# Kernel tuning notes

Measured on AMD Instinct MI355X. Metric: run time of the kernel, lower is better.

Reference implementation:

```python
import jax, jax.numpy as jnp
import numpy as np

N_NODES = 100000
N_EDGES = 100000
NNZ = 1600000


def setup_inputs() -> dict:
    key = jax.random.key(0)
    ks = jax.random.split(key, 6)
    x = jax.random.normal(ks[0], (N_NODES, 128), dtype=jnp.float32)
    hyperedge_index = jax.random.randint(ks[1], (2, NNZ), 0, N_EDGES, dtype=jnp.int64)
    # Glorot-ish init for linear weights, zero bias (PyG HypergraphConv lin + bias)
    W1 = jax.random.normal(ks[2], (128, 128), dtype=jnp.float32) / np.sqrt(128.0)
    b1 = jnp.zeros((128,), dtype=jnp.float32)
    W2 = jax.random.normal(ks[3], (128, 64), dtype=jnp.float32) / np.sqrt(128.0)
    b2 = jnp.zeros((64,), dtype=jnp.float32)
    return {"x": x, "hyperedge_index": hyperedge_index, "W1": W1, "b1": b1, "W2": W2, "b2": b2}


def _hypergraph_conv(x, node_idx, edge_idx, W, b):
    """PyG HypergraphConv (no attention, unit hyperedge weights):
    out = D^{-1} H B^{-1} H^T (x W) + b, with D = node degree, B = hyperedge degree."""
    x = x @ W  # [N, F]
    ones = jnp.ones((node_idx.shape[0],), dtype=x.dtype)
    deg_v = jax.ops.segment_sum(ones, node_idx, num_segments=N_NODES)   # D
    deg_e = jax.ops.segment_sum(ones, edge_idx, num_segments=N_EDGES)   # B
    d_inv = jnp.where(deg_v > 0, 1.0 / deg_v, 0.0)
    b_inv = jnp.where(deg_e > 0, 1.0 / deg_e, 0.0)
    # node -> hyperedge: m_e = B_e^{-1} * sum_{v in e} x_v
    m_e = jax.ops.segment_sum(x[node_idx], edge_idx, num_segments=N_EDGES) * b_inv[:, None]
    # hyperedge -> node: out_v = D_v^{-1} * sum_{e ∋ v} m_e
    out = jax.ops.segment_sum(m_e[edge_idx], node_idx, num_segments=N_NODES) * d_inv[:, None]
    return out + b


def reference(x, hyperedge_index, W1, b1, W2, b2):
    node_idx = hyperedge_index[0]
    edge_idx = hyperedge_index[1]
    h = _hypergraph_conv(x, node_idx, edge_idx, W1, b1)
    h = jax.nn.relu(h)
    # dropout is identity in eval mode (training=False)
    out = _hypergraph_conv(h, node_idx, edge_idx, W2, b2)
    return out
```

## Files before the change

kernel.cpp:

```cpp
#include <hip/hip_runtime.h>

#define NODES 100000
#define EDGES 100000
#define NNZV  1600000
#define NBK   196
#define BKCAP 12288
#define TILE2 2048
#define NTIL2 782

typedef unsigned short u16;
typedef __attribute__((ext_vector_type(8))) short bf16x8;
typedef __attribute__((ext_vector_type(4))) float f32x4;

__device__ __forceinline__ float b2f(u16 h) {
  union { unsigned u; float f; } c; c.u = ((unsigned)h) << 16; return c.f;
}
__device__ __forceinline__ u16 f2b(float f) {
  union { unsigned u; float f; } c; c.f = f;
  unsigned u = c.u + 0x7FFF + ((c.u >> 16) & 1);
  return (u16)(u >> 16);
}

__global__ __launch_bounds__(256) void wtrans_kernel(const float* __restrict__ W1,
                                                     const float* __restrict__ W2,
                                                     u16* __restrict__ W1T, u16* __restrict__ W2T) {
  int i = blockIdx.x * 256 + threadIdx.x;
  if (i < 16384) {
    int k = i >> 7, n = i & 127;
    W1T[n * 128 + k] = f2b(W1[i]);
  } else if (i < 16384 + 8192) {
    int j = i - 16384;
    int k = j >> 6, n = j & 63;
    W2T[n * 128 + k] = f2b(W2[j]);
  }
}

__global__ __launch_bounds__(256) void partition_kernel(const int* __restrict__ nidx,
                                                        const int* __restrict__ eidx,
                                                        int* __restrict__ gcnt,
                                                        unsigned* __restrict__ bk) {
  __shared__ int lcnt_e[NBK], lcnt_n[NBK], lbase_e[NBK], lbase_n[NBK];
  const int tid = threadIdx.x;
  const int j0 = blockIdx.x * TILE2;
  for (int i = tid; i < NBK; i += 256) { lcnt_e[i] = 0; lcnt_n[i] = 0; }
  __syncthreads();
  int be[8], bn[8]; unsigned pe[8], pn[8];
  #pragma unroll
  for (int i = 0; i < 8; i++) {
    int j = j0 + tid + i * 256;
    if (j < NNZV) {
      int e = __builtin_nontemporal_load(eidx + j);
      int n = __builtin_nontemporal_load(nidx + j);
      be[i] = e >> 9; pe[i] = ((unsigned)(e & 511) << 17) | (unsigned)n;
      bn[i] = n >> 9; pn[i] = ((unsigned)(n & 511) << 17) | (unsigned)e;
      atomicAdd(&lcnt_e[be[i]], 1);
      atomicAdd(&lcnt_n[bn[i]], 1);
    } else { be[i] = -1; bn[i] = -1; }
  }
  __syncthreads();
  for (int b = tid; b < NBK; b += 256) {
    int c = lcnt_e[b];
    lbase_e[b] = c ? atomicAdd(&gcnt[b], c) : 0;
    lcnt_e[b] = 0;
    c = lcnt_n[b];
    lbase_n[b] = c ? atomicAdd(&gcnt[NBK + b], c) : 0;
    lcnt_n[b] = 0;
  }
  __syncthreads();
  #pragma unroll
  for (int i = 0; i < 8; i++) {
    if (be[i] >= 0) {
      int p = lbase_e[be[i]] + atomicAdd(&lcnt_e[be[i]], 1);
      if (p < BKCAP) bk[(size_t)be[i] * BKCAP + p] = pe[i];
      p = lbase_n[bn[i]] + atomicAdd(&lcnt_n[bn[i]], 1);
      if (p < BKCAP) bk[(size_t)(NBK + bn[i]) * BKCAP + p] = pn[i];
    }
  }
}

__global__ __launch_bounds__(512) void bucket_sort_kernel(const int* __restrict__ gcnt,
                                                          const unsigned* __restrict__ bk,
                                                          int* __restrict__ off_e, int* __restrict__ off_v,
                                                          int* __restrict__ col_e, int* __restrict__ col_v) {
  const int gb = blockIdx.x;
  const int dir = gb >= NBK ? 1 : 0;
  const int b = dir ? gb - NBK : gb;
  const int* __restrict__ cnt = gcnt + dir * NBK;
  const unsigned* __restrict__ bkd = bk + ((size_t)dir * NBK + b) * BKCAP;
  int* __restrict__ off = dir ? off_v : off_e;
  int* __restrict__ col = dir ? col_v : col_e;
  const int tid = threadIdx.x, lane = tid & 63, wid = tid >> 6;
  __shared__ int lcnt[512];
  __shared__ int wsum[8];
  __shared__ int base_s;
  if (tid < 64) {
    int s = 0;
    for (int t = tid; t < b; t += 64) s += cnt[t];
    #pragma unroll
    for (int d = 1; d < 64; d <<= 1) s += __shfl_xor(s, d);
    if (tid == 0) base_s = s;
  }
  lcnt[tid] = 0;
  __syncthreads();
  const int n = min(cnt[b], BKCAP);
  for (int i = tid; i < n; i += 512)
    atomicAdd(&lcnt[bkd[i] >> 17], 1);
  __syncthreads();
  int x = lcnt[tid];
  int inc = x;
  #pragma unroll
  for (int d = 1; d < 64; d <<= 1) { int t = __shfl_up(inc, d); if (lane >= d) inc += t; }
  if (lane == 63) wsum[wid] = inc;
  __syncthreads();
  int wbase = 0;
  for (int k = 0; k < wid; k++) wbase += wsum[k];
  const int gpos = base_s + wbase + inc - x;
  const int row = (b << 9) + tid;
  if (row < NODES) off[row] = gpos;
  if (b == NBK - 1 && tid == 0) off[NODES] = NNZV;
  __syncthreads();
  lcnt[tid] = gpos;
  __syncthreads();
  for (int i = tid; i < n; i += 512) {
    unsigned e = bkd[i];
    int p = atomicAdd(&lcnt[e >> 17], 1);
    col[p] = (int)(e & 0x1FFFFu);
  }
}

template<int N, bool XBF>
__global__ __launch_bounds__(256) void gemm_kernel(const void* __restrict__ Xv,
                                                   const u16* __restrict__ WT,
                                                   u16* __restrict__ Y, int M) {
  __shared__ u16 sX[64 * 136];
  __shared__ u16 sW[N * 136];
  const int tid = threadIdx.x, lane = tid & 63, w = tid >> 6;
  const int chunk = blockIdx.x * 64;
  constexpr int WV = N * 128 / 8;
  for (int t = tid; t < WV; t += 256) {
    int e = t * 8, n = e >> 7, k = e & 127;
    *(bf16x8*)(sW + n * 136 + k) = *(const bf16x8*)(WT + n * 128 + k);
  }
  if constexpr (XBF) {
    const u16* X = (const u16*)Xv;
    for (int t = tid; t < 1024; t += 256) {
      int e = t * 8, r = e >> 7, k = e & 127;
      int row = min(chunk + r, M - 1);
      *(bf16x8*)(sX + r * 136 + k) = *(const bf16x8*)(X + (size_t)row * 128 + k);
    }
  } else {
    const float* X = (const float*)Xv;
    for (int t = tid; t < 2048; t += 256) {
      int r = t >> 5, c4 = t & 31;
      int row = min(chunk + r, M - 1);
      float4 v = *(const float4*)(X + (size_t)row * 128 + c4 * 4);
      ushort4 o = { f2b(v.x), f2b(v.y), f2b(v.z), f2b(v.w) };
      *(ushort4*)(sX + r * 136 + c4 * 4) = o;
    }
  }
  __syncthreads();
  constexpr int CW = N / 2;
  constexpr int NT = CW / 16;
  const int wr = w >> 1, wc = w & 1;
  const int l15 = lane & 15;
  const int arow = wr * 32 + l15;
  const int kb = (lane >> 4) * 8;
  f32x4 acc[2][NT];
  #pragma unroll
  for (int rt = 0; rt < 2; rt++)
    #pragma unroll
    for (int nt = 0; nt < NT; nt++) acc[rt][nt] = (f32x4){0.f, 0.f, 0.f, 0.f};
  #pragma unroll
  for (int kk = 0; kk < 4; kk++) {
    const int ko = kk * 32 + kb;
    bf16x8 a0 = *(const bf16x8*)(sX + arow * 136 + ko);
    bf16x8 a1 = *(const bf16x8*)(sX + (arow + 16) * 136 + ko);
    #pragma unroll
    for (int nt = 0; nt < NT; nt++) {
      bf16x8 bb = *(const bf16x8*)(sW + (wc * CW + nt * 16 + l15) * 136 + ko);
      acc[0][nt] = __builtin_amdgcn_mfma_f32_16x16x32_bf16(a0, bb, acc[0][nt], 0, 0, 0);
      acc[1][nt] = __builtin_amdgcn_mfma_f32_16x16x32_bf16(a1, bb, acc[1][nt], 0, 0, 0);
    }
  }
  const int r4 = (lane >> 4) * 4;
  #pragma unroll
  for (int rt = 0; rt < 2; rt++)
    #pragma unroll
    for (int r = 0; r < 4; r++) {
      int row = chunk + wr * 32 + rt * 16 + r4 + r;
      if (row < M) {
        #pragma unroll
        for (int nt = 0; nt < NT; nt++)
          Y[(size_t)row * N + wc * CW + nt * 16 + l15] = f2b(acc[rt][nt][r]);
      }
    }
}

template<int F, bool HASB, bool RELU, bool DSTBF>
__global__ __launch_bounds__(256) void gather_kernel(const int* __restrict__ off,
                                                     const int* __restrict__ col,
                                                     const u16* __restrict__ src,
                                                     const float* __restrict__ bias,
                                                     void* __restrict__ dstv, int nrows) {
  constexpr int G = (F == 128) ? 4 : 8;
  constexpr int L = 64 / G;
  const int row = blockIdx.x * 4 + (threadIdx.x >> 6);
  if (row >= nrows) return;
  const int lane = threadIdx.x & 63;
  const int g = lane / L;
  const int l = lane % L;
  const int s0 = off[row], s1 = off[row + 1];
  float acc[8] = {};
  int k = s0;
  for (; k + 4 * G <= s1; k += 4 * G) {
    int c0 = col[k + g];
    int c1 = col[k + G + g];
    int c2 = col[k + 2 * G + g];
    int c3 = col[k + 3 * G + g];
    bf16x8 v0 = *(const bf16x8*)(src + (size_t)c0 * F + l * 8);
    bf16x8 v1 = *(const bf16x8*)(src + (size_t)c1 * F + l * 8);
    bf16x8 v2 = *(const bf16x8*)(src + (size_t)c2 * F + l * 8);
    bf16x8 v3 = *(const bf16x8*)(src + (size_t)c3 * F + l * 8);
    #pragma unroll
    for (int t = 0; t < 8; t++) acc[t] += b2f((u16)v0[t]);
    #pragma unroll
    for (int t = 0; t < 8; t++) acc[t] += b2f((u16)v1[t]);
    #pragma unroll
    for (int t = 0; t < 8; t++) acc[t] += b2f((u16)v2[t]);
    #pragma unroll
    for (int t = 0; t < 8; t++) acc[t] += b2f((u16)v3[t]);
  }
  for (; k < s1; k += G) {
    int idx = k + g;
    int c = col[min(idx, s1 - 1)];
    bf16x8 v = *(const bf16x8*)(src + (size_t)c * F + l * 8);
    if (idx < s1) {
      #pragma unroll
      for (int t = 0; t < 8; t++) acc[t] += b2f((u16)v[t]);
    }
  }
  #pragma unroll
  for (int d = L; d < 64; d <<= 1) {
    #pragma unroll
    for (int t = 0; t < 8; t++) acc[t] += __shfl_xor(acc[t], d);
  }
  if (g == 0) {
    const float sc = (s1 > s0) ? 1.0f / (float)(s1 - s0) : 0.f;
    float v[8];
    #pragma unroll
    for (int t = 0; t < 8; t++) {
      v[t] = acc[t] * sc;
      if constexpr (HASB) v[t] += bias[l * 8 + t];
      if constexpr (RELU) v[t] = fmaxf(v[t], 0.f);
    }
    if constexpr (DSTBF) {
      bf16x8 o;
      #pragma unroll
      for (int t = 0; t < 8; t++) o[t] = (short)f2b(v[t]);
      *(bf16x8*)((u16*)dstv + (size_t)row * F + l * 8) = o;
    } else {
      float* d = (float*)dstv + (size_t)row * F + l * 8;
      *(float4*)d = make_float4(v[0], v[1], v[2], v[3]);
      *(float4*)(d + 4) = make_float4(v[4], v[5], v[6], v[7]);
    }
  }
}

extern "C" void kernel_launch(void* const* d_in, const int* in_sizes, int n_in,
                              void* d_out, int out_size, void* d_ws, size_t ws_size,
                              hipStream_t stream) {
  const float* x  = (const float*)d_in[0];
  const int*   hi = (const int*)d_in[1];
  const float* W1 = (const float*)d_in[2];
  const float* b1 = (const float*)d_in[3];
  const float* W2 = (const float*)d_in[4];
  const float* b2 = (const float*)d_in[5];
  float* out = (float*)d_out;
  const int* nidx = hi;
  const int* eidx = hi + NNZV;

  char* w = (char*)d_ws;
  int*      off_e = (int*)w;
  int*      off_v = (int*)(w + 524288);
  int*      gcnt  = (int*)(w + 1048576);
  u16*      W1T   = (u16*)(w + 1052672);
  u16*      W2T   = (u16*)(w + 1085440);
  int*      col_e = (int*)(w + 2097152);
  int*      col_v = (int*)(w + 8650752);
  unsigned* bk    = (unsigned*)(w + 16777216);
  u16*      bufH  = (u16*)(w + 56623104);
  u16*      bufM  = (u16*)(w + 56623104 + 25600000);

  hipMemsetAsync(gcnt, 0, 392 * 4, stream);
  wtrans_kernel<<<96, 256, 0, stream>>>(W1, W2, W1T, W2T);
  partition_kernel<<<NTIL2, 256, 0, stream>>>(nidx, eidx, gcnt, bk);
  bucket_sort_kernel<<<2 * NBK, 512, 0, stream>>>(gcnt, bk, off_e, off_v, col_e, col_v);

  gemm_kernel<128, false><<<1563, 256, 0, stream>>>(x, W1T, bufH, NODES);
  gather_kernel<128, false, false, true><<<(EDGES + 3) / 4, 256, 0, stream>>>(
      off_e, col_e, bufH, nullptr, bufM, EDGES);
  gather_kernel<128, true, true, true><<<(NODES + 3) / 4, 256, 0, stream>>>(
      off_v, col_v, bufM, b1, bufH, NODES);
  gemm_kernel<64, true><<<1563, 256, 0, stream>>>(bufH, W2T, bufM, NODES);
  gather_kernel<64, false, false, true><<<(EDGES + 3) / 4, 256, 0, stream>>>(
      off_e, col_e, bufM, nullptr, bufH, EDGES);
  gather_kernel<64, true, false, false><<<(NODES + 3) / 4, 256, 0, stream>>>(
      off_v, col_v, bufH, b2, out, NODES);
}
```

Before: 316.2 us.

## Slice feature matrices into column slabs and gather per slice for cache locality

Intermediate feature buffers are stored as 8 column slices (each slice holds all rows for F/8 features). GEMMs write and read in this sliced layout, and a new gather kernel assigns blockIdx%8 to a slice and runs a grid-stride loop over rows, 4 rows per wave. The aim is to keep each slice's working set (about 3.2MB or 1.6MB) resident in L2/LLC so random gathers hit cache instead of HBM. The cost is 8x re-reading of the CSR index arrays and narrower 8-byte loads per lane, partly offset by nontemporal loads and stores.

New measurement: 852.2 us. 2.69x slower.

```diff
diff --git a/kernel.cpp b/kernel.cpp
--- a/kernel.cpp
+++ b/kernel.cpp
@@ -2,15 +2,18 @@
 
 #define NODES 100000
 #define EDGES 100000
+#define NR    100000
 #define NNZV  1600000
 #define NBK   196
 #define BKCAP 12288
 #define TILE2 2048
 #define NTIL2 782
+#define NBGS  512
 
 typedef unsigned short u16;
 typedef __attribute__((ext_vector_type(8))) short bf16x8;
 typedef __attribute__((ext_vector_type(4))) float f32x4;
+typedef __attribute__((ext_vector_type(4))) unsigned short u16x4;
 
 __device__ __forceinline__ float b2f(u16 h) {
   union { unsigned u; float f; } c; c.u = ((unsigned)h) << 16; return c.f;
@@ -128,7 +131,7 @@
   }
 }
 
-template<int N, bool XBF>
+template<int N, bool XBF, int OS>
 __global__ __launch_bounds__(256) void gemm_kernel(const void* __restrict__ Xv,
                                                    const u16* __restrict__ WT,
                                                    u16* __restrict__ Y, int M) {
@@ -144,9 +147,12 @@
   if constexpr (XBF) {
     const u16* X = (const u16*)Xv;
     for (int t = tid; t < 1024; t += 256) {
-      int e = t * 8, r = e >> 7, k = e & 127;
+      int ss = t >> 7;
+      int u = t & 127;
+      int r = u >> 1, half = u & 1;
       int row = min(chunk + r, M - 1);
-      *(bf16x8*)(sX + r * 136 + k) = *(const bf16x8*)(X + (size_t)row * 128 + k);
+      *(bf16x8*)(sX + r * 136 + ss * 16 + half * 8) =
+          *(const bf16x8*)(X + (size_t)ss * NR * 16 + (size_t)row * 16 + half * 8);
     }
   } else {
     const float* X = (const float*)Xv;
@@ -190,78 +196,100 @@
       int row = chunk + wr * 32 + rt * 16 + r4 + r;
       if (row < M) {
         #pragma unroll
-        for (int nt = 0; nt < NT; nt++)
-          Y[(size_t)row * N + wc * CW + nt * 16 + l15] = f2b(acc[rt][nt][r]);
+        for (int nt = 0; nt < NT; nt++) {
+          int cn = wc * CW + nt * 16 + l15;
+          int sl = cn / OS, fi = cn % OS;
+          Y[(size_t)sl * NR * OS + (size_t)row * OS + fi] = f2b(acc[rt][nt][r]);
+        }
       }
     }
 }
 
-template<int F, bool HASB, bool RELU, bool DSTBF>
-__global__ __launch_bounds__(256) void gather_kernel(const int* __restrict__ off,
-                                                     const int* __restrict__ col,
-                                                     const u16* __restrict__ src,
-                                                     const float* __restrict__ bias,
-                                                     void* __restrict__ dstv, int nrows) {
-  constexpr int G = (F == 128) ? 4 : 8;
-  constexpr int L = 64 / G;
-  const int row = blockIdx.x * 4 + (threadIdx.x >> 6);
-  if (row >= nrows) return;
-  const int lane = threadIdx.x & 63;
-  const int g = lane / L;
-  const int l = lane % L;
-  const int s0 = off[row], s1 = off[row + 1];
-  float acc[8] = {};
-  int k = s0;
-  for (; k + 4 * G <= s1; k += 4 * G) {
-    int c0 = col[k + g];
-    int c1 = col[k + G + g];
-    int c2 = col[k + 2 * G + g];
-    int c3 = col[k + 3 * G + g];
-    bf16x8 v0 = *(const bf16x8*)(src + (size_t)c0 * F + l * 8);
-    bf16x8 v1 = *(const bf16x8*)(src + (size_t)c1 * F + l * 8);
-    bf16x8 v2 = *(const bf16x8*)(src + (size_t)c2 * F + l * 8);
-    bf16x8 v3 = *(const bf16x8*)(src + (size_t)c3 * F + l * 8);
-    #pragma unroll
-    for (int t = 0; t < 8; t++) acc[t] += b2f((u16)v0[t]);
-    #pragma unroll
-    for (int t = 0; t < 8; t++) acc[t] += b2f((u16)v1[t]);
-    #pragma unroll
-    for (int t = 0; t < 8; t++) acc[t] += b2f((u16)v2[t]);
-    #pragma unroll
-    for (int t = 0; t < 8; t++) acc[t] += b2f((u16)v3[t]);
-  }
-  for (; k < s1; k += G) {
-    int idx = k + g;
-    int c = col[min(idx, s1 - 1)];
-    bf16x8 v = *(const bf16x8*)(src + (size_t)c * F + l * 8);
-    if (idx < s1) {
+template<int F, bool HASB, bool RELU, bool F32OUT>
+__global__ __launch_bounds__(256) void gatherS_kernel(const int* __restrict__ off,
+                                                      const int* __restrict__ col,
+                                                      const u16* __restrict__ src,
+                                                      const float* __restrict__ bias,
+                                                      void* __restrict__ dstv, int nrows) {
+  constexpr int SLICE = F / 8;
+  constexpr int LPM   = SLICE / 4;
+  constexpr int SLOTS = 64 / LPM;
+  constexpr int NB0   = (F == 128) ? 2 : 1;
+  const int s = blockIdx.x & 7;
+  const int b = blockIdx.x >> 3;
+  const int lane = threadIdx.x & 63, wave = threadIdx.x >> 6;
+  const int g = lane / LPM;
+  const int l = lane % LPM;
+  const u16* __restrict__ srcS = src + (size_t)s * NR * SLICE;
+  float bi[4];
+  if constexpr (HASB) {
+    #pragma unroll
+    for (int t = 0; t < 4; t++) bi[t] = bias[s * SLICE + l * 4 + t];
+  }
+  for (int row0 = b * 16 + wave * 4; row0 < nrows; row0 += NBGS * 16) {
+    int s0a[4], s1a[4];
+    #pragma unroll
+    for (int rr = 0; rr < 4; rr++) {
+      int row = row0 + rr;
+      s0a[rr] = (row < nrows) ? off[row] : 0;
+      s1a[rr] = (row < nrows) ? off[row + 1] : 0;
+    }
+    float acc[4][4] = {};
+    #pragma unroll
+    for (int bb = 0; bb < NB0; bb++) {
+      int ia[4]; ushort4 va[4];
       #pragma unroll
-      for (int t = 0; t < 8; t++) acc[t] += b2f((u16)v[t]);
-    }
-  }
-  #pragma unroll
-  for (int d = L; d < 64; d <<= 1) {
-    #pragma unroll
-    for (int t = 0; t < 8; t++) acc[t] += __shfl_xor(acc[t], d);
-  }
-  if (g == 0) {
-    const float sc = (s1 > s0) ? 1.0f / (float)(s1 - s0) : 0.f;
-    float v[8];
-    #pragma unroll
-    for (int t = 0; t < 8; t++) {
-      v[t] = acc[t] * sc;
-      if constexpr (HASB) v[t] += bias[l * 8 + t];
-      if constexpr (RELU) v[t] = fmaxf(v[t], 0.f);
-    }
-    if constexpr (DSTBF) {
-      bf16x8 o;
+      for (int rr = 0; rr < 4; rr++) {
+        ia[rr] = s0a[rr] + bb * SLOTS + g;
+        int c = __builtin_nontemporal_load(col + min(ia[rr], NNZV - 1));
+        va[rr] = *(const ushort4*)(srcS + (size_t)c * SLICE + l * 4);
+      }
       #pragma unroll
-      for (int t = 0; t < 8; t++) o[t] = (short)f2b(v[t]);
-      *(bf16x8*)((u16*)dstv + (size_t)row * F + l * 8) = o;
-    } else {
-      float* d = (float*)dstv + (size_t)row * F + l * 8;
-      *(float4*)d = make_float4(v[0], v[1], v[2], v[3]);
-      *(float4*)(d + 4) = make_float4(v[4], v[5], v[6], v[7]);
+      for (int rr = 0; rr < 4; rr++)
+        if (ia[rr] < s1a[rr]) {
+          acc[rr][0] += b2f(va[rr].x); acc[rr][1] += b2f(va[rr].y);
+          acc[rr][2] += b2f(va[rr].z); acc[rr][3] += b2f(va[rr].w);
+        }
+    }
+    #pragma unroll
+    for (int rr = 0; rr < 4; rr++) {
+      for (int k = s0a[rr] + NB0 * SLOTS; k < s1a[rr]; k += SLOTS) {
+        int idx = k + g;
+        int c = __builtin_nontemporal_load(col + min(idx, NNZV - 1));
+        ushort4 v = *(const ushort4*)(srcS + (size_t)c * SLICE + l * 4);
+        if (idx < s1a[rr]) {
+          acc[rr][0] += b2f(v.x); acc[rr][1] += b2f(v.y);
+          acc[rr][2] += b2f(v.z); acc[rr][3] += b2f(v.w);
+        }
+      }
+    }
+    #pragma unroll
+    for (int rr = 0; rr < 4; rr++)
+      #pragma unroll
+      for (int d = LPM; d < 64; d <<= 1)
+        #pragma unroll
+        for (int t = 0; t < 4; t++) acc[rr][t] += __shfl_xor(acc[rr][t], d);
+    if (g == 0) {
+      #pragma unroll
+      for (int rr = 0; rr < 4; rr++) {
+        int row = row0 + rr;
+        if (row >= nrows) continue;
+        const float sc = (s1a[rr] > s0a[rr]) ? 1.0f / (float)(s1a[rr] - s0a[rr]) : 0.f;
+        float v[4];
+        #pragma unroll
+        for (int t = 0; t < 4; t++) {
+          v[t] = acc[rr][t] * sc;
+          if constexpr (HASB) v[t] += bi[t];
+          if constexpr (RELU) v[t] = fmaxf(v[t], 0.f);
+        }
+        if constexpr (F32OUT) {
+          f32x4 o = {v[0], v[1], v[2], v[3]};
+          __builtin_nontemporal_store(o, (f32x4*)((float*)dstv + (size_t)row * 64 + s * 8 + l * 4));
+        } else {
+          u16x4 o = {f2b(v[0]), f2b(v[1]), f2b(v[2]), f2b(v[3])};
+          __builtin_nontemporal_store(o, (u16x4*)((u16*)dstv + (size_t)s * NR * SLICE + (size_t)row * SLICE + l * 4));
+        }
+      }
     }
   }
 }
@@ -296,14 +324,14 @@
   partition_kernel<<<NTIL2, 256, 0, stream>>>(nidx, eidx, gcnt, bk);
   bucket_sort_kernel<<<2 * NBK, 512, 0, stream>>>(gcnt, bk, off_e, off_v, col_e, col_v);
 
-  gemm_kernel<128, false><<<1563, 256, 0, stream>>>(x, W1T, bufH, NODES);
-  gather_kernel<128, false, false, true><<<(EDGES + 3) / 4, 256, 0, stream>>>(
+  gemm_kernel<128, false, 16><<<1563, 256, 0, stream>>>(x, W1T, bufH, NODES);
+  gatherS_kernel<128, false, false, false><<<8 * NBGS, 256, 0, stream>>>(
       off_e, col_e, bufH, nullptr, bufM, EDGES);
-  gather_kernel<128, true, true, true><<<(NODES + 3) / 4, 256, 0, stream>>>(
+  gatherS_kernel<128, true, true, false><<<8 * NBGS, 256, 0, stream>>>(
       off_v, col_v, bufM, b1, bufH, NODES);
-  gemm_kernel<64, true><<<1563, 256, 0, stream>>>(bufH, W2T, bufM, NODES);
-  gather_kernel<64, false, false, true><<<(EDGES + 3) / 4, 256, 0, stream>>>(
+  gemm_kernel<64, true, 8><<<1563, 256, 0, stream>>>(bufH, W2T, bufM, NODES);
+  gatherS_kernel<64, false, false, false><<<8 * NBGS, 256, 0, stream>>>(
       off_e, col_e, bufM, nullptr, bufH, EDGES);
-  gather_kernel<64, true, false, false><<<(NODES + 3) / 4, 256, 0, stream>>>(
+  gatherS_kernel<64, true, false, true><<<8 * NBGS, 256, 0, stream>>>(
       off_v, col_v, bufH, b2, out, NODES);
 }
```
